# Performance work log

Measured on AMD Instinct MI355X. Metric: run time of the kernel, lower is better.

Reference implementation:

```python
import jax, jax.numpy as jnp
import numpy as np

NU, NV, D, H, R, B = 4096, 4096, 256, 64, 5, 4096


def setup_inputs() -> dict:
    key = jax.random.key(0)
    ks = jax.random.split(key, 8)
    xav = (2.0 / (D + H)) ** 0.5  # xavier_normal std for [D,H] weights
    return {
        "u_feat": jax.random.normal(ks[0], (NU, D), jnp.float32),
        "v_feat": jax.random.normal(ks[1], (NV, D), jnp.float32),
        "u": jax.random.randint(ks[2], (B,), 0, NU),
        "v": jax.random.randint(ks[3], (B,), 0, NV),
        "support": jax.random.uniform(ks[4], (R, NU, NV), jnp.float32),
        "u_weight": jax.random.normal(ks[5], (R, D, H), jnp.float32) * xav,
        "v_weight": jax.random.normal(ks[6], (R, D, H), jnp.float32) * xav,
        "u_bias": jax.random.normal(ks[7], (H,), jnp.float32),
    }


def _sym_norm(support):
    # normalize(): diag(rowsum(mx,1)^-0.5) @ mx @ diag(colsum(mx,0)^-0.5),
    # expressed as broadcasted per-row / per-col scaling (no dense diag matmul).
    col = support.sum(axis=1)  # [R, NV] (torch.sum(mx, 0))
    row = support.sum(axis=2)  # [R, NU] (torch.sum(mx, 1))
    r_inv = jnp.where(col > 0, jax.lax.rsqrt(jnp.where(col > 0, col, 1.0)), 0.0)
    c_inv = jnp.where(row > 0, jax.lax.rsqrt(jnp.where(row > 0, row, 1.0)), 0.0)
    return support * c_inv[:, :, None] * r_inv[:, None, :]  # [R, NU, NV]
    # note: normalize(support[r].T) == _sym_norm(support)[r].T (symmetric scaling)


def reference(u_feat, v_feat, u, v, support, u_weight, v_weight, u_bias):
    # per-relation weight accumulation: w_r_eff = sum_{r'<=r} w_{r'}
    uw = jnp.cumsum(u_weight, axis=0)  # [R, D, H]
    vw = jnp.cumsum(v_weight, axis=0)
    tmp_u = jnp.einsum('nd,rdh->rnh', u_feat, uw)  # [R, NU, H]
    tmp_v = jnp.einsum('md,rdh->rmh', v_feat, vw)  # [R, NV, H]
    sn = _sym_norm(support)  # [R, NU, NV]
    # gather selected user rows / item columns, contract, sum over relations
    z_u = jnp.einsum('rbm,rmh->bh', sn[:, u, :], tmp_v) + u_bias  # [B, H]
    z_v = jnp.einsum('rnb,rnh->bh', sn[:, :, v], tmp_u) + u_bias  # [B, H]
    return jax.nn.relu(z_u), jax.nn.relu(z_v)
```

## Files before the change

kernel.cpp:

```cpp
#include <hip/hip_runtime.h>
#include <stdint.h>

#define NU 4096
#define NV 4096
#define DD 256
#define HH 64
#define RR 5

typedef _Float16 f16x8 __attribute__((ext_vector_type(8)));
typedef float f32x4 __attribute__((ext_vector_type(4)));

__device__ __forceinline__ uint16_t f16bits(float f) {
  union { _Float16 h; uint16_t u; } cv;
  cv.h = (_Float16)f;
  return cv.u;
}

__device__ __forceinline__ f16x8 cvt8(const float* p) {
  float4 a = *(const float4*)p;
  float4 b = *(const float4*)(p + 4);
  f16x8 r;
  r[0] = (_Float16)a.x; r[1] = (_Float16)a.y; r[2] = (_Float16)a.z; r[3] = (_Float16)a.w;
  r[4] = (_Float16)b.x; r[5] = (_Float16)b.y; r[6] = (_Float16)b.z; r[7] = (_Float16)b.w;
  return r;
}


__device__ __forceinline__ void stage_f32(const float* g, char* ldsT, int lane, int gstride) {
  int sub = lane >> 3;
  int s7  = lane & 7;
  f16x8 vals[8];
  #pragma unroll
  for (int c = 0; c < 8; c++)
    vals[c] = cvt8(g + (size_t)(c * 8 + sub) * gstride + s7 * 8);
  #pragma unroll
  for (int c = 0; c < 8; c++) {
    int row = c * 8 + sub;
    int slot = row * 8 + (s7 ^ sub ^ c);
    *(f16x8*)(ldsT + slot * 16) = vals[c];
  }
}

__device__ __forceinline__ void stage_f16(const _Float16* g, char* ldsT, int lane, int gstride) {
  int sub = lane >> 3;
  int s7  = lane & 7;
  f16x8 vals[8];
  #pragma unroll
  for (int c = 0; c < 8; c++)
    vals[c] = *(const f16x8*)(g + (size_t)(c * 8 + sub) * gstride + s7 * 8);
  #pragma unroll
  for (int c = 0; c < 8; c++) {
    int slot = (c * 8 + sub) * 8 + (s7 ^ sub ^ c);
    *(f16x8*)(ldsT + slot * 16) = vals[c];
  }
}

__device__ __forceinline__ void stage_transpose_f32(const float* g, char* ldsT, int lane, int gstride) {
  int moct = lane & 7;
  int noct = lane >> 3;
  uint16_t hv[8][8];
  #pragma unroll
  for (int j = 0; j < 8; j++) {
    const float* p = g + (size_t)(noct * 8 + j) * gstride + moct * 8;
    float4 a = *(const float4*)p;
    float4 b = *(const float4*)(p + 4);
    hv[j][0] = f16bits(a.x); hv[j][1] = f16bits(a.y); hv[j][2] = f16bits(a.z); hv[j][3] = f16bits(a.w);
    hv[j][4] = f16bits(b.x); hv[j][5] = f16bits(b.y); hv[j][6] = f16bits(b.z); hv[j][7] = f16bits(b.w);
  }
  #pragma unroll
  for (int jm = 0; jm < 8; jm++) {
    uint4 o;
    o.x = (uint32_t)hv[0][jm] | ((uint32_t)hv[1][jm] << 16);
    o.y = (uint32_t)hv[2][jm] | ((uint32_t)hv[3][jm] << 16);
    o.z = (uint32_t)hv[4][jm] | ((uint32_t)hv[5][jm] << 16);
    o.w = (uint32_t)hv[6][jm] | ((uint32_t)hv[7][jm] << 16);
    int m = moct * 8 + jm;
    int slot = m * 8 + (noct ^ (m & 7) ^ ((m >> 3) & 7));
    *(uint4*)(ldsT + slot * 16) = o;
  }
}

__device__ __forceinline__ void mfma_tile64(const char* ldsA, const char* ldsB,
                                            f32x4 acc[4][4], int lane) {
  int rowl = lane & 15;
  int q = lane >> 4;
  #pragma unroll
  for (int ks = 0; ks < 2; ks++) {
    int koct = ks * 4 + q;
    f16x8 af[4], bfr[4];
    #pragma unroll
    for (int mt = 0; mt < 4; mt++) {
      int row = mt * 16 + rowl;
      int slot = row * 8 + (koct ^ (row & 7) ^ ((row >> 3) & 7));
      af[mt] = *(const f16x8*)(ldsA + slot * 16);
    }
    #pragma unroll
    for (int ht = 0; ht < 4; ht++) {
      int row = ht * 16 + rowl;
      int slot = row * 8 + (koct ^ (row & 7) ^ ((row >> 3) & 7));
      bfr[ht] = *(const f16x8*)(ldsB + slot * 16);
    }
    #pragma unroll
    for (int mt = 0; mt < 4; mt++)
      #pragma unroll
      for (int ht = 0; ht < 4; ht++)
        acc[mt][ht] = __builtin_amdgcn_mfma_f32_16x16x32_f16(af[mt], bfr[ht], acc[mt][ht], 0, 0, 0);
  }
}

__global__ __launch_bounds__(256) void k_zero(float* __restrict__ p) {
  p[blockIdx.x * 256 + threadIdx.x] = 0.f;
}

__global__ __launch_bounds__(256) void k_sums(const float* __restrict__ S,
                                              float* __restrict__ rowsum,
                                              float* __restrict__ colsum) {
  int r = blockIdx.x >> 7;
  int chunk = blockIdx.x & 127;
  int n0 = chunk * 32;
  int t = threadIdx.x;
  const float* base = S + (size_t)r * NU * NV;
  float colacc[16];
  #pragma unroll
  for (int j = 0; j < 16; j++) colacc[j] = 0.f;
  for (int nr = 0; nr < 32; nr++) {
    const float* row = base + (size_t)(n0 + nr) * NV;
    float rp = 0.f;
    #pragma unroll
    for (int j = 0; j < 4; j++) {
      float4 v = *(const float4*)(row + j * 1024 + t * 4);
      rp += v.x + v.y + v.z + v.w;
      colacc[j * 4 + 0] += v.x; colacc[j * 4 + 1] += v.y;
      colacc[j * 4 + 2] += v.z; colacc[j * 4 + 3] += v.w;
    }
    #pragma unroll
    for (int off = 32; off > 0; off >>= 1) rp += __shfl_xor(rp, off, 64);
    if ((t & 63) == 0) atomicAdd(&rowsum[r * NU + n0 + nr], rp);
  }
  #pragma unroll
  for (int j = 0; j < 4; j++)
    #pragma unroll
    for (int i = 0; i < 4; i++)
      atomicAdd(&colsum[r * NV + j * 1024 + t * 4 + i], colacc[j * 4 + i]);
}

__global__ __launch_bounds__(256) void k_inv(const float* __restrict__ sums,
                                             float* __restrict__ invs) {
  int i = blockIdx.x * 256 + threadIdx.x;
  float v = sums[i];
  invs[i] = v > 0.f ? rsqrtf(v) : 0.f;
}

__global__ __launch_bounds__(256) void k_wt(const float* __restrict__ uw,
                                            const float* __restrict__ vw,
                                            _Float16* __restrict__ wtu,
                                            _Float16* __restrict__ wtv) {
  int r = blockIdx.x % RR;
  const float* w = (blockIdx.x < RR) ? uw : vw;
  _Float16* o = (blockIdx.x < RR) ? wtu : wtv;
  int t = threadIdx.x;
  for (int h = 0; h < HH; h++) {
    float s = 0.f;
    for (int rp = 0; rp <= r; rp++) s += w[rp * DD * HH + t * HH + h];
    o[(size_t)(r * HH + h) * DD + t] = (_Float16)s;
  }
}

__global__ __launch_bounds__(128) void k_tmp(const float* __restrict__ u_feat,
                                             const float* __restrict__ v_feat,
                                             const _Float16* __restrict__ wtu,
                                             const _Float16* __restrict__ wtv,
                                             const float* __restrict__ invs,
                                             _Float16* __restrict__ TuT,
                                             _Float16* __restrict__ TvT) {
  __shared__ __align__(16) char lds[32768];
  int bx = blockIdx.x, r = blockIdx.y, dir = blockIdx.z;
  int t = threadIdx.x, w = t >> 6, lane = t & 63;
  char* ldsA = lds + w * 16384;
  char* ldsB = ldsA + 8192;
  const float* feat = dir ? v_feat : u_feat;
  const _Float16* wt = dir ? wtv : wtu;
  const float* inv = invs + (dir ? (size_t)RR * NU : 0);
  _Float16* outT = dir ? TvT : TuT;
  int n0 = bx * 64;
  f32x4 acc[4][4];
  #pragma unroll
  for (int a = 0; a < 4; a++)
    #pragma unroll
    for (int b = 0; b < 4; b++) acc[a][b] = (f32x4){0.f, 0.f, 0.f, 0.f};
  #pragma unroll
  for (int cc = 0; cc < 2; cc++) {
    int kw = (w * 2 + cc) * 64;
    stage_f32(feat + (size_t)n0 * DD + kw, ldsA, lane, DD);
    stage_f16(wt + (size_t)(r * HH) * DD + kw, ldsB, lane, DD);
    mfma_tile64(ldsA, ldsB, acc, lane);
  }
  {
    float* slab = (float*)ldsA;
    int rowl = lane & 15, q = lane >> 4;
    #pragma unroll
    for (int mt = 0; mt < 4; mt++)
      #pragma unroll
      for (int ht = 0; ht < 4; ht++)
        #pragma unroll
        for (int i = 0; i < 4; i++)
          slab[(mt * 16 + q * 4 + i) * 64 + ht * 16 + rowl] = acc[mt][ht][i];
  }
  __syncthreads();
  {
    int h = t & 63, rg = t >> 6;
    uint32_t pk[16];
    #pragma unroll
    for (int p = 0; p < 16; p++) {
      int rl = rg * 32 + 2 * p;
      float s0 = ((const float*)lds)[rl * 64 + h] + ((const float*)(lds + 16384))[rl * 64 + h];
      float s1 = ((const float*)lds)[(rl + 1) * 64 + h] + ((const float*)(lds + 16384))[(rl + 1) * 64 + h];
      s0 *= inv[r * NU + n0 + rl];
      s1 *= inv[r * NU + n0 + rl + 1];
      pk[p] = (uint32_t)f16bits(s0) | ((uint32_t)f16bits(s1) << 16);
    }
    uint32_t* ob = (uint32_t*)(outT + ((size_t)(r * HH + h) * NU + n0 + rg * 32));
    #pragma unroll
    for (int p = 0; p < 16; p++) ob[p] = pk[p];
  }
}

__global__ __launch_bounds__(128) void k_gemm(const float* __restrict__ S,
                                              const _Float16* __restrict__ TuT,
                                              const _Float16* __restrict__ TvT,
                                              const float* __restrict__ invs,
                                              float* __restrict__ Yu,
                                              float* __restrict__ Yv) {
  __shared__ __align__(16) char lds[32768];
  int bx = blockIdx.x, r = blockIdx.y, dir = blockIdx.z;
  int mtile = bx & 63, khalf = bx >> 6;
  int t = threadIdx.x, w = t >> 6, lane = t & 63;
  char* ldsA = lds + w * 16384;
  char* ldsB = ldsA + 8192;
  const float* Sr = S + (size_t)r * NU * NV;
  const _Float16* Tb = (dir ? TuT : TvT) + (size_t)r * HH * NV;
  const float* inv = invs + (dir ? (size_t)RR * NU : 0) + (size_t)r * NU;
  float* Yo = (dir ? Yv : Yu) + (size_t)mtile * 64 * HH;
  int row0 = mtile * 64;
  f32x4 acc[4][4];
  #pragma unroll
  for (int a = 0; a < 4; a++)
    #pragma unroll
    for (int b = 0; b < 4; b++) acc[a][b] = (f32x4){0.f, 0.f, 0.f, 0.f};
  for (int ch = 0; ch < 16; ch++) {
    int k0 = khalf * 2048 + w * 1024 + ch * 64;
    if (dir == 0) {
      stage_f32(Sr + (size_t)row0 * NV + k0, ldsA, lane, NV);
    } else {
      stage_transpose_f32(Sr + (size_t)k0 * NV + row0, ldsA, lane, NV);
    }
    stage_f16(Tb + k0, ldsB, lane, NV);
    mfma_tile64(ldsA, ldsB, acc, lane);
  }
  {
    float* slab = (float*)ldsA;
    int rowl = lane & 15, q = lane >> 4;
    #pragma unroll
    for (int mt = 0; mt < 4; mt++)
      #pragma unroll
      for (int ht = 0; ht < 4; ht++)
        #pragma unroll
        for (int i = 0; i < 4; i++)
          slab[(mt * 16 + q * 4 + i) * 64 + ht * 16 + rowl] = acc[mt][ht][i];
  }
  __syncthreads();
  {
    int h = t & 63, rg = t >> 6;
    #pragma unroll
    for (int j = 0; j < 32; j++) {
      int row = rg * 32 + j;
      float s = ((const float*)lds)[row * 64 + h] + ((const float*)(lds + 16384))[row * 64 + h];
      atomicAdd(&Yo[(size_t)row * HH + h], s * inv[row0 + row]);
    }
  }
}

__global__ __launch_bounds__(256) void k_out(const int* __restrict__ u, const int* __restrict__ v,
                                             const float* __restrict__ Yu, const float* __restrict__ Yv,
                                             const float* __restrict__ bias,
                                             float* __restrict__ out) {
  int T = blockIdx.x * 256 + threadIdx.x;
  int dir = T >> 17;
  int rem = T & 131071;
  int b = rem >> 5;
  int h = (rem & 31) * 2;
  int idx = dir ? v[b] : u[b];
  const float* Y = (dir ? Yv : Yu) + (size_t)idx * HH + h;
  float s0 = Y[0] + bias[h];
  float s1 = Y[1] + bias[h + 1];
  float2 o;
  o.x = s0 > 0.f ? s0 : 0.f;
  o.y = s1 > 0.f ? s1 : 0.f;
  ((float2*)out)[T] = o;
}

extern "C" void kernel_launch(void* const* d_in, const int* in_sizes, int n_in,
                              void* d_out, int out_size, void* d_ws, size_t ws_size,
                              hipStream_t stream) {
  (void)in_sizes; (void)n_in; (void)out_size; (void)ws_size;
  const float* u_feat = (const float*)d_in[0];
  const float* v_feat = (const float*)d_in[1];
  const int* u = (const int*)d_in[2];
  const int* v = (const int*)d_in[3];
  const float* S = (const float*)d_in[4];
  const float* uw = (const float*)d_in[5];
  const float* vw = (const float*)d_in[6];
  const float* bias = (const float*)d_in[7];

  char* ws = (char*)d_ws;
  float* sums = (float*)ws;
  float* Yu   = (float*)(ws + 163840);
  float* Yv   = (float*)(ws + 1212416);
  float* invs = (float*)(ws + 2260992);
  _Float16* wtu = (_Float16*)(ws + 2424832);
  _Float16* wtv = (_Float16*)(ws + 2588672);
  _Float16* TuT = (_Float16*)(ws + 2752512);
  _Float16* TvT = (_Float16*)(ws + 5373952);

  k_zero<<<2208, 256, 0, stream>>>(sums);
  k_wt<<<2 * RR, 256, 0, stream>>>(uw, vw, wtu, wtv);
  k_sums<<<RR * 128, 256, 0, stream>>>(S, sums, sums + (size_t)RR * NU);
  k_inv<<<160, 256, 0, stream>>>(sums, invs);
  k_tmp<<<dim3(64, RR, 2), 128, 0, stream>>>(u_feat, v_feat, wtu, wtv, invs, TuT, TvT);
  k_gemm<<<dim3(128, RR, 2), 128, 0, stream>>>(S, TuT, TvT, invs, Yu, Yv);
  k_out<<<1024, 256, 0, stream>>>(u, v, Yu, Yv, bias, (float*)d_out);
}
```

Before: 686.9 us.

## Convert support to fp16 during sum pass and stream fp16 in GEMM

The row/column-sum kernel now also writes an fp16 copy of the support tensor, and the GEMM kernel reads that copy for both directions instead of re-reading fp32 twice. This halves the bytes the GEMM pulls from memory and removes conversion work from the transposed staging path, at the cost of an extra large write in the prep pass. The weight cumulative-sum kernel is also parallelised across many more blocks.

```diff
diff --git a/kernel.cpp b/kernel.cpp
--- a/kernel.cpp
+++ b/kernel.cpp
@@ -8,6 +8,7 @@
 #define RR 5
 
 typedef _Float16 f16x8 __attribute__((ext_vector_type(8)));
+typedef _Float16 f16x4 __attribute__((ext_vector_type(4)));
 typedef float f32x4 __attribute__((ext_vector_type(4)));
 
 __device__ __forceinline__ uint16_t f16bits(float f) {
@@ -55,25 +56,24 @@
   }
 }
 
-__device__ __forceinline__ void stage_transpose_f32(const float* g, char* ldsT, int lane, int gstride) {
+__device__ __forceinline__ void stage_transpose_f16(const _Float16* g, char* ldsT, int lane, int gstride) {
   int moct = lane & 7;
   int noct = lane >> 3;
-  uint16_t hv[8][8];
+  uint32_t rw[8][4];
   #pragma unroll
   for (int j = 0; j < 8; j++) {
-    const float* p = g + (size_t)(noct * 8 + j) * gstride + moct * 8;
-    float4 a = *(const float4*)p;
-    float4 b = *(const float4*)(p + 4);
-    hv[j][0] = f16bits(a.x); hv[j][1] = f16bits(a.y); hv[j][2] = f16bits(a.z); hv[j][3] = f16bits(a.w);
-    hv[j][4] = f16bits(b.x); hv[j][5] = f16bits(b.y); hv[j][6] = f16bits(b.z); hv[j][7] = f16bits(b.w);
+    uint4 vv = *(const uint4*)(g + (size_t)(noct * 8 + j) * gstride + moct * 8);
+    rw[j][0] = vv.x; rw[j][1] = vv.y; rw[j][2] = vv.z; rw[j][3] = vv.w;
   }
   #pragma unroll
   for (int jm = 0; jm < 8; jm++) {
     uint4 o;
-    o.x = (uint32_t)hv[0][jm] | ((uint32_t)hv[1][jm] << 16);
-    o.y = (uint32_t)hv[2][jm] | ((uint32_t)hv[3][jm] << 16);
-    o.z = (uint32_t)hv[4][jm] | ((uint32_t)hv[5][jm] << 16);
-    o.w = (uint32_t)hv[6][jm] | ((uint32_t)hv[7][jm] << 16);
+    #define XTR(J) ((rw[J][jm >> 1] >> ((jm & 1) * 16)) & 0xFFFFu)
+    o.x = XTR(0) | (XTR(1) << 16);
+    o.y = XTR(2) | (XTR(3) << 16);
+    o.z = XTR(4) | (XTR(5) << 16);
+    o.w = XTR(6) | (XTR(7) << 16);
+    #undef XTR
     int m = moct * 8 + jm;
     int slot = m * 8 + (noct ^ (m & 7) ^ ((m >> 3) & 7));
     *(uint4*)(ldsT + slot * 16) = o;
@@ -112,7 +112,8 @@
   p[blockIdx.x * 256 + threadIdx.x] = 0.f;
 }
 
-__global__ __launch_bounds__(256) void k_sums(const float* __restrict__ S,
+__global__ __launch_bounds__(256) void k_prep(const float* __restrict__ S,
+                                              _Float16* __restrict__ Sh,
                                               float* __restrict__ rowsum,
                                               float* __restrict__ colsum) {
   int r = blockIdx.x >> 7;
@@ -120,11 +121,13 @@
   int n0 = chunk * 32;
   int t = threadIdx.x;
   const float* base = S + (size_t)r * NU * NV;
+  _Float16* hbase = Sh + (size_t)r * NU * NV;
   float colacc[16];
   #pragma unroll
   for (int j = 0; j < 16; j++) colacc[j] = 0.f;
   for (int nr = 0; nr < 32; nr++) {
     const float* row = base + (size_t)(n0 + nr) * NV;
+    _Float16* hrow = hbase + (size_t)(n0 + nr) * NV;
     float rp = 0.f;
     #pragma unroll
     for (int j = 0; j < 4; j++) {
@@ -132,6 +135,10 @@
       rp += v.x + v.y + v.z + v.w;
       colacc[j * 4 + 0] += v.x; colacc[j * 4 + 1] += v.y;
       colacc[j * 4 + 2] += v.z; colacc[j * 4 + 3] += v.w;
+      f16x4 hv;
+      hv[0] = (_Float16)v.x; hv[1] = (_Float16)v.y;
+      hv[2] = (_Float16)v.z; hv[3] = (_Float16)v.w;
+      *(f16x4*)(hrow + j * 1024 + t * 4) = hv;
     }
     #pragma unroll
     for (int off = 32; off > 0; off >>= 1) rp += __shfl_xor(rp, off, 64);
@@ -155,15 +162,16 @@
                                             const float* __restrict__ vw,
                                             _Float16* __restrict__ wtu,
                                             _Float16* __restrict__ wtv) {
-  int r = blockIdx.x % RR;
-  const float* w = (blockIdx.x < RR) ? uw : vw;
-  _Float16* o = (blockIdx.x < RR) ? wtu : wtv;
-  int t = threadIdx.x;
-  for (int h = 0; h < HH; h++) {
-    float s = 0.f;
-    for (int rp = 0; rp <= r; rp++) s += w[rp * DD * HH + t * HH + h];
-    o[(size_t)(r * HH + h) * DD + t] = (_Float16)s;
-  }
+  int r = blockIdx.y, side = blockIdx.z;
+  int e = blockIdx.x * 256 + threadIdx.x;
+  int d = e >> 6, h = e & 63;
+  const float* w = side ? vw : uw;
+  _Float16* o = side ? wtv : wtu;
+  float s = 0.f;
+  #pragma unroll
+  for (int rp = 0; rp < RR; rp++)
+    if (rp <= r) s += w[rp * DD * HH + e];
+  o[(size_t)(r * HH + h) * DD + d] = (_Float16)s;
 }
 
 __global__ __launch_bounds__(128) void k_tmp(const float* __restrict__ u_feat,
@@ -225,7 +233,7 @@
   }
 }
 
-__global__ __launch_bounds__(128) void k_gemm(const float* __restrict__ S,
+__global__ __launch_bounds__(128) void k_gemm(const _Float16* __restrict__ Sh,
                                               const _Float16* __restrict__ TuT,
                                               const _Float16* __restrict__ TvT,
                                               const float* __restrict__ invs,
@@ -237,7 +245,7 @@
   int t = threadIdx.x, w = t >> 6, lane = t & 63;
   char* ldsA = lds + w * 16384;
   char* ldsB = ldsA + 8192;
-  const float* Sr = S + (size_t)r * NU * NV;
+  const _Float16* Sr = Sh + (size_t)r * NU * NV;
   const _Float16* Tb = (dir ? TuT : TvT) + (size_t)r * HH * NV;
   const float* inv = invs + (dir ? (size_t)RR * NU : 0) + (size_t)r * NU;
   float* Yo = (dir ? Yv : Yu) + (size_t)mtile * 64 * HH;
@@ -250,9 +258,9 @@
   for (int ch = 0; ch < 16; ch++) {
     int k0 = khalf * 2048 + w * 1024 + ch * 64;
     if (dir == 0) {
-      stage_f32(Sr + (size_t)row0 * NV + k0, ldsA, lane, NV);
+      stage_f16(Sr + (size_t)row0 * NV + k0, ldsA, lane, NV);
     } else {
-      stage_transpose_f32(Sr + (size_t)k0 * NV + row0, ldsA, lane, NV);
+      stage_transpose_f16(Sr + (size_t)k0 * NV + row0, ldsA, lane, NV);
     }
     stage_f16(Tb + k0, ldsB, lane, NV);
     mfma_tile64(ldsA, ldsB, acc, lane);
@@ -321,12 +329,13 @@
   _Float16* wtv = (_Float16*)(ws + 2588672);
   _Float16* TuT = (_Float16*)(ws + 2752512);
   _Float16* TvT = (_Float16*)(ws + 5373952);
+  _Float16* Sh  = (_Float16*)(ws + 7995392);
 
   k_zero<<<2208, 256, 0, stream>>>(sums);
-  k_wt<<<2 * RR, 256, 0, stream>>>(uw, vw, wtu, wtv);
-  k_sums<<<RR * 128, 256, 0, stream>>>(S, sums, sums + (size_t)RR * NU);
+  k_wt<<<dim3(64, RR, 2), 256, 0, stream>>>(uw, vw, wtu, wtv);
+  k_prep<<<RR * 128, 256, 0, stream>>>(S, Sh, sums, sums + (size_t)RR * NU);
   k_inv<<<160, 256, 0, stream>>>(sums, invs);
   k_tmp<<<dim3(64, RR, 2), 128, 0, stream>>>(u_feat, v_feat, wtu, wtv, invs, TuT, TvT);
-  k_gemm<<<dim3(128, RR, 2), 128, 0, stream>>>(S, TuT, TvT, invs, Yu, Yv);
+  k_gemm<<<dim3(128, RR, 2), 128, 0, stream>>>(Sh, TuT, TvT, invs, Yu, Yv);
   k_out<<<1024, 256, 0, stream>>>(u, v, Yu, Yv, bias, (float*)d_out);
 }
```

New measurement: 602.2 us. 12.3% less time.
